# Optimization experiments

Hardware: AMD Instinct MI355X
Metric: run time of the kernel (lower is better)

Reference implementation:

```python
import jax, jax.numpy as jnp
import numpy as np

B, S, D, H = 2, 2048, 1024, 16
DK = D // H
EPS = 1e-5


def setup_inputs() -> dict:
    key = jax.random.key(0)
    ks = jax.random.split(key, 6)
    std = (2.0 / (D + D)) ** 0.5
    return {
        "x": jax.random.normal(ks[0], (B, S, D), dtype=jnp.float32),
        "W_Q": jax.random.normal(ks[1], (D, D), dtype=jnp.float32) * std,
        "W_K": jax.random.normal(ks[2], (D, D), dtype=jnp.float32) * std,
        "W_V": jax.random.normal(ks[3], (D, D), dtype=jnp.float32) * std,
        "W_O": jax.random.normal(ks[4], (D, D), dtype=jnp.float32) * std,
        "gain": jnp.ones((D,), dtype=jnp.float32),
        "positions": jnp.arange(S, dtype=jnp.int64 if jax.config.jax_enable_x64 else jnp.int32),
        "theta": 10000,
        "max_seq_len": 2048,
    }


def rmsnorm(x, gain):
    xf = x.astype(jnp.float32)
    rms = jnp.sqrt(jnp.mean(xf * xf, axis=-1, keepdims=True) + EPS)
    return ((xf / rms) * gain).astype(x.dtype)


def apply_rope(x, sin, cos):
    # x: [..., seq, dk]; sin/cos: [seq, dk//2] broadcast over leading dims
    x_even = x[..., 0::2]
    x_odd = x[..., 1::2]
    r_even = x_even * cos - x_odd * sin
    r_odd = x_odd * cos + x_even * sin
    return jnp.stack([r_even, r_odd], axis=-1).reshape(x.shape)


def reference(x, W_Q, W_K, W_V, W_O, gain, positions, theta, max_seq_len):
    seq_len = x.shape[-2]
    Q = jnp.einsum('od,bsd->bso', W_Q, x)
    K = jnp.einsum('od,bsd->bso', W_K, x)
    V = jnp.einsum('od,bsd->bso', W_V, x)
    # RMSNorm over full d_model BEFORE head split (as in original)
    Q = rmsnorm(Q, gain)
    K = rmsnorm(K, gain)
    # split heads: [b, h, s, dk]
    Q = Q.reshape(*Q.shape[:-1], H, DK).swapaxes(-3, -2)
    K = K.reshape(*K.shape[:-1], H, DK).swapaxes(-3, -2)
    V = V.reshape(*V.shape[:-1], H, DK).swapaxes(-3, -2)
    # RoPE tables
    exponents = 2.0 * jnp.arange(DK // 2, dtype=jnp.float32) / DK
    inv_freq = 1.0 / (jnp.float32(theta) ** exponents)
    angles = positions.astype(jnp.float32)[:, None] * inv_freq[None, :]  # [S, DK//2]
    sin, cos = jnp.sin(angles), jnp.cos(angles)
    Q = apply_rope(Q, sin, cos)
    K = apply_rope(K, sin, cos)
    # causal attention
    scores = jnp.einsum('bhqd,bhkd->bhqk', Q, K) / jnp.sqrt(jnp.float32(DK))
    causal = jnp.tril(jnp.ones((seq_len, seq_len), dtype=bool))
    scores = jnp.where(causal, scores, -jnp.inf)
    attn = jax.nn.softmax(scores, axis=-1)
    out = jnp.einsum('bhqk,bhkd->bhqd', attn, V)
    out = out.swapaxes(-3, -2).reshape(*x.shape[:-1], D)
    return jnp.einsum('of,bsf->bso', W_O, out)
```

## Files before the change

### kernel.cpp

```cpp
#include <hip/hip_runtime.h>
#include <hip/hip_bf16.h>

typedef __attribute__((ext_vector_type(8))) __bf16 bf16x8;
typedef __attribute__((ext_vector_type(4))) __bf16 bf16x4;
typedef __attribute__((ext_vector_type(4))) float  f32x4;

#define S_LEN 2048
#define D_DIM 1024
#define NH    16
#define GK    1024
#define GN    1024

__device__ __forceinline__ float fast_exp2(float x) {
#if __has_builtin(__builtin_amdgcn_exp2f)
  return __builtin_amdgcn_exp2f(x);
#else
  return exp2f(x);
#endif
}

__device__ __forceinline__ void gld_lds16(const void* g, void* l) {
  __builtin_amdgcn_global_load_lds(
      (const __attribute__((address_space(1))) unsigned int*)g,
      (__attribute__((address_space(3))) unsigned int*)l, 16, 0, 0);
}

__global__ __launch_bounds__(256) void cast_all(
    const float* __restrict__ x,  const float* __restrict__ wq, const float* __restrict__ wk,
    const float* __restrict__ wv, const float* __restrict__ wo,
    __bf16* __restrict__ xb, __bf16* __restrict__ wqb, __bf16* __restrict__ wkb,
    __bf16* __restrict__ wvb, __bf16* __restrict__ wob)
{
  const int NTOT = 2 << 20;
  for (int i = blockIdx.x * 256 + threadIdx.x; i < NTOT; i += 1024 * 256) {
    const float* s; __bf16* d; int off;
    if (i < (1 << 20)) { s = x; d = xb; off = i; }
    else {
      const int j = i - (1 << 20);
      const int r = j >> 18; off = j & ((1 << 18) - 1);
      s = (r == 0) ? wq : (r == 1) ? wk : (r == 2) ? wv : wo;
      d = (r == 0) ? wqb : (r == 1) ? wkb : (r == 2) ? wvb : wob;
    }
    float4 v = ((const float4*)s)[off];
    bf16x4 o = { (__bf16)v.x, (__bf16)v.y, (__bf16)v.z, (__bf16)v.w };
    ((bf16x4*)d)[off] = o;
  }
}

__global__ __launch_bounds__(256) void gemm_bt(
    const __bf16* __restrict__ A,
    const __bf16* __restrict__ W0, const __bf16* __restrict__ W1, const __bf16* __restrict__ W2,
    __bf16* __restrict__ C0, __bf16* __restrict__ C1, __bf16* __restrict__ VtOut)
{
  const int mode = blockIdx.z;
  const __bf16* Wm = (mode == 0) ? W0 : (mode == 1) ? W1 : W2;

  __shared__ __align__(16) __bf16 As[128 * 64];
  __shared__ __align__(16) __bf16 Bs[128 * 64];

  const int tid  = threadIdx.x;
  const int lane = tid & 63;
  const int w    = tid >> 6;
  const int wr   = w >> 1, wc = w & 1;
  const int lm   = lane & 15, qd = lane >> 4;
  const int m0 = blockIdx.y * 128, n0 = blockIdx.x * 128;

  const __bf16* ap[4]; const __bf16* bp[4]; int lo[4];
  #pragma unroll
  for (int j = 0; j < 4; j++) {
    const int c = tid + 256 * j;
    const int r = c >> 3, cpos = c & 7;
    const int g = (cpos ^ (r & 7)) * 8;
    ap[j] = A  + (size_t)(m0 + r) * GK + g;
    bp[j] = Wm + (size_t)(n0 + r) * GK + g;
    lo[j] = c * 8;
  }

  const int sw = lm & 7;

  f32x4 zero = {0.f, 0.f, 0.f, 0.f};
  f32x4 acc[4][4];
  #pragma unroll
  for (int i = 0; i < 4; i++)
    #pragma unroll
    for (int j = 0; j < 4; j++) acc[i][j] = zero;

  for (int k0 = 0; k0 < GK; k0 += 64) {
    #pragma unroll
    for (int j = 0; j < 4; j++) {
      gld_lds16(ap[j] + k0, &As[lo[j]]);
      gld_lds16(bp[j] + k0, &Bs[lo[j]]);
    }
    __syncthreads();
    #pragma unroll
    for (int half = 0; half < 2; half++) {
      const int cph = ((qd + 4 * half) ^ sw) * 8;
      bf16x8 af[4], bfv[4];
      #pragma unroll
      for (int i = 0; i < 4; i++) af[i]  = *(const bf16x8*)&As[(wr * 64 + i * 16 + lm) * 64 + cph];
      #pragma unroll
      for (int j = 0; j < 4; j++) bfv[j] = *(const bf16x8*)&Bs[(wc * 64 + j * 16 + lm) * 64 + cph];
      #pragma unroll
      for (int i = 0; i < 4; i++)
        #pragma unroll
        for (int j = 0; j < 4; j++)
          acc[i][j] = __builtin_amdgcn_mfma_f32_16x16x32_bf16(af[i], bfv[j], acc[i][j], 0, 0, 0);
    }
    __syncthreads();
  }

  if (mode < 2) {
    __bf16* C = (mode == 0) ? C0 : C1;
    #pragma unroll
    for (int i = 0; i < 4; i++) {
      const int row = m0 + wr * 64 + i * 16 + qd * 4;
      #pragma unroll
      for (int j = 0; j < 4; j++) {
        const int col = n0 + wc * 64 + j * 16 + lm;
        #pragma unroll
        for (int r = 0; r < 4; r++)
          C[(size_t)(row + r) * GN + col] = (__bf16)acc[i][j][r];
      }
    }
  } else {
    #pragma unroll
    for (int i = 0; i < 4; i++) {
      const int row = m0 + wr * 64 + i * 16 + qd * 4;
      const int b = row >> 11, s = row & (S_LEN - 1);
      #pragma unroll
      for (int j = 0; j < 4; j++) {
        const int col = n0 + wc * 64 + j * 16 + lm;
        const int h = col >> 6, d = col & 63;
        bf16x4 o = { (__bf16)acc[i][j][0], (__bf16)acc[i][j][1],
                     (__bf16)acc[i][j][2], (__bf16)acc[i][j][3] };
        *(bf16x4*)(VtOut + (((size_t)(b * NH + h) * 64 + d) * S_LEN + s)) = o;
      }
    }
  }
}

__global__ __launch_bounds__(256) void gemm_out64(
    const __bf16* __restrict__ A, const __bf16* __restrict__ Wm, float* __restrict__ C)
{
  __shared__ __align__(16) __bf16 As[64 * 64];
  __shared__ __align__(16) __bf16 Bs[128 * 64];

  const int tid  = threadIdx.x;
  const int lane = tid & 63;
  const int w    = tid >> 6;
  const int wr   = w >> 1, wc = w & 1;
  const int lm   = lane & 15, qd = lane >> 4;
  const int m0 = blockIdx.y * 64, n0 = blockIdx.x * 128;

  const __bf16* ap[2]; int loA[2];
  #pragma unroll
  for (int j = 0; j < 2; j++) {
    const int c = tid + 256 * j;
    const int r = c >> 3, cpos = c & 7;
    ap[j] = A + (size_t)(m0 + r) * GK + (cpos ^ (r & 7)) * 8;
    loA[j] = c * 8;
  }
  const __bf16* bp[4]; int loB[4];
  #pragma unroll
  for (int j = 0; j < 4; j++) {
    const int c = tid + 256 * j;
    const int r = c >> 3, cpos = c & 7;
    bp[j] = Wm + (size_t)(n0 + r) * GK + (cpos ^ (r & 7)) * 8;
    loB[j] = c * 8;
  }

  const int sw = lm & 7;

  f32x4 zero = {0.f, 0.f, 0.f, 0.f};
  f32x4 acc[2][4];
  #pragma unroll
  for (int i = 0; i < 2; i++)
    #pragma unroll
    for (int j = 0; j < 4; j++) acc[i][j] = zero;

  for (int k0 = 0; k0 < GK; k0 += 64) {
    #pragma unroll
    for (int j = 0; j < 2; j++) gld_lds16(ap[j] + k0, &As[loA[j]]);
    #pragma unroll
    for (int j = 0; j < 4; j++) gld_lds16(bp[j] + k0, &Bs[loB[j]]);
    __syncthreads();
    #pragma unroll
    for (int half = 0; half < 2; half++) {
      const int cph = ((qd + 4 * half) ^ sw) * 8;
      bf16x8 af[2], bfv[4];
      #pragma unroll
      for (int i = 0; i < 2; i++) af[i]  = *(const bf16x8*)&As[(wr * 32 + i * 16 + lm) * 64 + cph];
      #pragma unroll
      for (int j = 0; j < 4; j++) bfv[j] = *(const bf16x8*)&Bs[(wc * 64 + j * 16 + lm) * 64 + cph];
      #pragma unroll
      for (int i = 0; i < 2; i++)
        #pragma unroll
        for (int j = 0; j < 4; j++)
          acc[i][j] = __builtin_amdgcn_mfma_f32_16x16x32_bf16(af[i], bfv[j], acc[i][j], 0, 0, 0);
    }
    __syncthreads();
  }

  #pragma unroll
  for (int i = 0; i < 2; i++) {
    const int row = m0 + wr * 32 + i * 16 + qd * 4;
    #pragma unroll
    for (int j = 0; j < 4; j++) {
      const int col = n0 + wc * 64 + j * 16 + lm;
      #pragma unroll
      for (int r = 0; r < 4; r++)
        C[(size_t)(row + r) * GN + col] = acc[i][j][r];
    }
  }
}

__global__ __launch_bounds__(256) void norm_rope(
    const __bf16* __restrict__ Qf, const __bf16* __restrict__ Kf,
    const float* __restrict__ gain, const int* __restrict__ positions,
    const int* __restrict__ theta_p,
    __bf16* __restrict__ Qh, __bf16* __restrict__ Kh)
{
  const int row = blockIdx.x;
  const int s = row & (S_LEN - 1), b = row >> 11;
  const int t = threadIdx.x, d0 = t * 4;

  const bf16x4 qv = *(const bf16x4*)(Qf + (size_t)row * D_DIM + d0);
  const bf16x4 kv = *(const bf16x4*)(Kf + (size_t)row * D_DIM + d0);
  const float q0 = (float)qv[0], q1 = (float)qv[1], q2 = (float)qv[2], q3 = (float)qv[3];
  const float k0 = (float)kv[0], k1 = (float)kv[1], k2 = (float)kv[2], k3 = (float)kv[3];

  float sq = q0 * q0 + q1 * q1 + q2 * q2 + q3 * q3;
  float sk = k0 * k0 + k1 * k1 + k2 * k2 + k3 * k3;
  #pragma unroll
  for (int off = 32; off; off >>= 1) { sq += __shfl_xor(sq, off); sk += __shfl_xor(sk, off); }
  __shared__ float red[8];
  const int lane = t & 63, wv = t >> 6;
  if (lane == 0) { red[wv] = sq; red[4 + wv] = sk; }
  __syncthreads();
  sq = red[0] + red[1] + red[2] + red[3];
  sk = red[4] + red[5] + red[6] + red[7];
  const float invq = rsqrtf(sq * (1.0f / 1024.0f) + 1e-5f);
  const float invk = rsqrtf(sk * (1.0f / 1024.0f) + 1e-5f);

  const float4 g = *(const float4*)(gain + d0);
  const float qn0 = q0 * invq * g.x, qn1 = q1 * invq * g.y;
  const float qn2 = q2 * invq * g.z, qn3 = q3 * invq * g.w;
  const float kn0 = k0 * invk * g.x, kn1 = k1 * invk * g.y;
  const float kn2 = k2 * invk * g.z, kn3 = k3 * invk * g.w;

  const float pos = (float)positions[s];
  const float th  = (float)theta_p[0];
  const int idx = d0 & 63, h = d0 >> 6, p0 = idx >> 1;
  const float lg32 = __log2f(th) * (1.0f / 32.0f);
  const float f0 = fast_exp2(-(float)p0 * lg32);
  const float f1 = fast_exp2(-(float)(p0 + 1) * lg32);
  float s0, cc0, s1, cc1;
  __sincosf(pos * f0, &s0, &cc0);
  __sincosf(pos * f1, &s1, &cc1);

  const float qe0 = qn0 * cc0 - qn1 * s0, qo0 = qn1 * cc0 + qn0 * s0;
  const float qe1 = qn2 * cc1 - qn3 * s1, qo1 = qn3 * cc1 + qn2 * s1;
  const float ke0 = kn0 * cc0 - kn1 * s0, ko0 = kn1 * cc0 + kn0 * s0;
  const float ke1 = kn2 * cc1 - kn3 * s1, ko1 = kn3 * cc1 + kn2 * s1;

  const size_t obase = ((size_t)((b * NH + h) * S_LEN + s)) * 64 + idx;
  bf16x4 qo = { (__bf16)qe0, (__bf16)qo0, (__bf16)qe1, (__bf16)qo1 };
  bf16x4 ko = { (__bf16)ke0, (__bf16)ko0, (__bf16)ke1, (__bf16)ko1 };
  *(bf16x4*)(Qh + obase) = qo;
  *(bf16x4*)(Kh + obase) = ko;
}

__global__ __launch_bounds__(256) void attn_fwd(
    const __bf16* __restrict__ Qh, const __bf16* __restrict__ Kh,
    const __bf16* __restrict__ Vt, __bf16* __restrict__ Ob)
{
  const int bid = blockIdx.x;
  const int g   = bid >> 5, gj = g & 7, gs = g >> 3;
  const int qt  = (gs == 0) ? 31 - gj : (gs == 1) ? gj : (gs == 2) ? 23 - gj : 8 + gj;
  const int rr  = bid & 31;
  const int bh  = (rr & 7) * 4 + (rr >> 3);
  const int tid = threadIdx.x, lane = tid & 63, w = tid >> 6;
  const int lm = lane & 15, qd = lane >> 4;

  __shared__ __align__(16) __bf16 smem[8192 + 8192 + 4096];
  __bf16* Ks = smem;
  __bf16* Vs = smem + 8192;
  __bf16* Pw = smem + 16384 + w * 1024;

  const int row0 = qt * 64 + w * 16;
  const size_t qbase = (size_t)bh * S_LEN * 64;
  const bf16x8 aq0 = *(const bf16x8*)(Qh + qbase + (size_t)(row0 + lm) * 64 + qd * 8);
  const bf16x8 aq1 = *(const bf16x8*)(Qh + qbase + (size_t)(row0 + lm) * 64 + 32 + qd * 8);

  const __bf16* Kb = Kh + (size_t)bh * S_LEN * 64;
  const __bf16* Vb = Vt + (size_t)bh * 64 * S_LEN;
  const int c0 = tid, c1 = 256 + tid;
  const int kr0 = c0 >> 3, kr1 = c1 >> 3;
  const int kg0 = ((c0 & 7) ^ (kr0 & 7)) * 8;
  const int kg1 = ((c1 & 7) ^ (kr1 & 7)) * 8;
  const int cpA = (qd ^ (lm & 7)) * 8;
  const int cpB = cpA ^ 32;

  auto stage = [&](int buf, int k0) {
    __bf16* Kd = Ks + buf * 4096;
    __bf16* Vd = Vs + buf * 4096;
    gld_lds16(Kb + (size_t)(k0 + kr0) * 64 + kg0, &Kd[c0 * 8]);
    gld_lds16(Kb + (size_t)(k0 + kr1) * 64 + kg1, &Kd[c1 * 8]);
    gld_lds16(Vb + (size_t)kr0 * S_LEN + k0 + kg0, &Vd[c0 * 8]);
    gld_lds16(Vb + (size_t)kr1 * S_LEN + k0 + kg1, &Vd[c1 * 8]);
  };

  const float SC2 = 0.125f * 1.44269504089f;
  const float OFF = 12.0f;
  f32x4 zero = {0.f, 0.f, 0.f, 0.f};
  float l[4] = {0.f, 0.f, 0.f, 0.f};
  f32x4 o[4];
  #pragma unroll
  for (int jb = 0; jb < 4; jb++) o[jb] = zero;

  stage(0, 0);

  const int rowg = row0 + qd * 4;
  const int pxor = qd * 4;

  for (int kt = 0; kt <= qt; ++kt) {
    const int cur = kt & 1;
    __syncthreads();
    if (kt < qt) stage(cur ^ 1, (kt + 1) * 64);

    const __bf16* Kc = Ks + cur * 4096;
    const __bf16* Vc = Vs + cur * 4096;
    const int k0 = kt * 64;

    float p[4][4];
    const bool diag = (kt == qt);
    #pragma unroll
    for (int kb = 0; kb < 4; kb++) {
      const int krow = (kb * 16 + lm) * 64;
      const bf16x8 bk0 = *(const bf16x8*)&Kc[krow + cpA];
      const bf16x8 bk1 = *(const bf16x8*)&Kc[krow + cpB];
      f32x4 sc = zero;
      sc = __builtin_amdgcn_mfma_f32_16x16x32_bf16(aq0, bk0, sc, 0, 0, 0);
      sc = __builtin_amdgcn_mfma_f32_16x16x32_bf16(aq1, bk1, sc, 0, 0, 0);
      if (diag) {
        const int colg = k0 + kb * 16 + lm;
        #pragma unroll
        for (int r = 0; r < 4; r++) {
          const float e = fast_exp2(fmaf(sc[r], SC2, -OFF));
          p[kb][r] = (colg <= rowg + r) ? e : 0.f;
          l[r] += p[kb][r];
        }
      } else {
        #pragma unroll
        for (int r = 0; r < 4; r++) {
          p[kb][r] = fast_exp2(fmaf(sc[r], SC2, -OFF));
          l[r] += p[kb][r];
        }
      }
    }

    #pragma unroll
    for (int kb = 0; kb < 4; kb++) {
      const int cb = kb * 2 + (lm >> 3), wi = lm & 7;
      #pragma unroll
      for (int r = 0; r < 4; r++) {
        const int prow = pxor + r;
        Pw[prow * 64 + ((cb ^ (prow & 7)) << 3) + wi] = (__bf16)p[kb][r];
      }
    }

    const bf16x8 ap0 = *(const bf16x8*)&Pw[lm * 64 + cpA];
    const bf16x8 ap1 = *(const bf16x8*)&Pw[lm * 64 + cpB];
    #pragma unroll
    for (int jb = 0; jb < 4; jb++) {
      const int vrow = (jb * 16 + lm) * 64;
      const bf16x8 bv0 = *(const bf16x8*)&Vc[vrow + cpA];
      const bf16x8 bv1 = *(const bf16x8*)&Vc[vrow + cpB];
      o[jb] = __builtin_amdgcn_mfma_f32_16x16x32_bf16(ap1, bv1,
              __builtin_amdgcn_mfma_f32_16x16x32_bf16(ap0, bv0, o[jb], 0, 0, 0), 0, 0, 0);
    }
  }

  const int b = bh >> 4, h = bh & 15;
  #pragma unroll
  for (int r = 0; r < 4; r++) {
    float lr = l[r];
    #pragma unroll
    for (int off = 8; off; off >>= 1) lr += __shfl_xor(lr, off);
    const float inv = 1.0f / lr;
    const size_t base = ((size_t)(b * S_LEN + rowg + r)) * D_DIM + h * 64;
    #pragma unroll
    for (int jb = 0; jb < 4; jb++)
      Ob[base + jb * 16 + lm] = (__bf16)(o[jb][r] * inv);
  }
}

extern "C" void kernel_launch(void* const* d_in, const int* in_sizes, int n_in,
                              void* d_out, int out_size, void* d_ws, size_t ws_size,
                              hipStream_t stream)
{
  (void)in_sizes; (void)n_in; (void)out_size; (void)ws_size;
  const float* x    = (const float*)d_in[0];
  const float* WQ   = (const float*)d_in[1];
  const float* WK   = (const float*)d_in[2];
  const float* WV   = (const float*)d_in[3];
  const float* WO   = (const float*)d_in[4];
  const float* gain = (const float*)d_in[5];
  const int* positions = (const int*)d_in[6];
  const int* theta     = (const int*)d_in[7];
  float* out = (float*)d_out;

  char* ws = (char*)d_ws;
  const size_t MB = 1024 * 1024;
  __bf16* xb  = (__bf16*)(ws + 0);
  __bf16* WQb = (__bf16*)(ws + 8  * MB);
  __bf16* WKb = (__bf16*)(ws + 10 * MB);
  __bf16* WVb = (__bf16*)(ws + 12 * MB);
  __bf16* WOb = (__bf16*)(ws + 14 * MB);
  __bf16* Qfb = (__bf16*)(ws + 16 * MB);
  __bf16* Kfb = (__bf16*)(ws + 24 * MB);
  __bf16* Vt  = (__bf16*)(ws + 32 * MB);
  __bf16* Qh  = (__bf16*)(ws + 40 * MB);
  __bf16* Kh  = (__bf16*)(ws + 48 * MB);
  __bf16* Ob  = (__bf16*)(ws + 56 * MB);

  cast_all<<<1024, 256, 0, stream>>>(x, WQ, WK, WV, WO, xb, WQb, WKb, WVb, WOb);
  gemm_bt<<<dim3(8, 32, 3), 256, 0, stream>>>(xb, WQb, WKb, WVb, Qfb, Kfb, Vt);
  norm_rope<<<4096, 256, 0, stream>>>(Qfb, Kfb, gain, positions, theta, Qh, Kh);
  attn_fwd<<<1024, 256, 0, stream>>>(Qh, Kh, Vt, Ob);
  gemm_out64<<<dim3(8, 64), 256, 0, stream>>>(Ob, WOb, out);
}
```

Baseline: 190.8 us.

## Shrink QKV GEMM tiles to 64x128 and remap blocks for XCD-aware L2 locality

The QKV projection GEMM now uses 64x128 tiles instead of 128x128, which doubles the block count to 1536 so more of the GPU's compute units are filled. Both GEMMs switch to a 1D grid where the low three bits of the block id pick a region of the output, so blocks that land on the same XCD tend to share rows of A and columns of W in L2. Launch bounds now ask for 6 blocks per CU to raise occupancy. The cost is lower arithmetic intensity per tile, meaning more LDS and global traffic per FLOP, and the occupancy hint may limit registers.

```diff
diff --git a/kernel.cpp b/kernel.cpp
--- a/kernel.cpp
+++ b/kernel.cpp
@@ -47,15 +47,21 @@
   }
 }
 
-__global__ __launch_bounds__(256) void gemm_bt(
+__global__ __launch_bounds__(256, 6) void gemm_qkv(
     const __bf16* __restrict__ A,
     const __bf16* __restrict__ W0, const __bf16* __restrict__ W1, const __bf16* __restrict__ W2,
     __bf16* __restrict__ C0, __bf16* __restrict__ C1, __bf16* __restrict__ VtOut)
 {
-  const int mode = blockIdx.z;
+  const int bid = blockIdx.x;
+  const int e = bid & 7, mg = e >> 1, ng = e & 1;
+  const int q = bid >> 3;
+  const int mode = q % 3;
+  const int t = q / 3;
+  const int m0 = (mg * 16 + (t & 15)) * 64;
+  const int n0 = (ng * 4 + (t >> 4)) * 128;
   const __bf16* Wm = (mode == 0) ? W0 : (mode == 1) ? W1 : W2;
 
-  __shared__ __align__(16) __bf16 As[128 * 64];
+  __shared__ __align__(16) __bf16 As[64 * 64];
   __shared__ __align__(16) __bf16 Bs[128 * 64];
 
   const int tid  = threadIdx.x;
@@ -63,45 +69,49 @@
   const int w    = tid >> 6;
   const int wr   = w >> 1, wc = w & 1;
   const int lm   = lane & 15, qd = lane >> 4;
-  const int m0 = blockIdx.y * 128, n0 = blockIdx.x * 128;
-
-  const __bf16* ap[4]; const __bf16* bp[4]; int lo[4];
+
+  const __bf16* ap[2]; int loA[2];
+  #pragma unroll
+  for (int j = 0; j < 2; j++) {
+    const int c = tid + 256 * j;
+    const int r = c >> 3, cpos = c & 7;
+    ap[j] = A + (size_t)(m0 + r) * GK + (cpos ^ (r & 7)) * 8;
+    loA[j] = c * 8;
+  }
+  const __bf16* bp[4]; int loB[4];
   #pragma unroll
   for (int j = 0; j < 4; j++) {
     const int c = tid + 256 * j;
     const int r = c >> 3, cpos = c & 7;
-    const int g = (cpos ^ (r & 7)) * 8;
-    ap[j] = A  + (size_t)(m0 + r) * GK + g;
-    bp[j] = Wm + (size_t)(n0 + r) * GK + g;
-    lo[j] = c * 8;
+    bp[j] = Wm + (size_t)(n0 + r) * GK + (cpos ^ (r & 7)) * 8;
+    loB[j] = c * 8;
   }
 
   const int sw = lm & 7;
 
   f32x4 zero = {0.f, 0.f, 0.f, 0.f};
-  f32x4 acc[4][4];
-  #pragma unroll
-  for (int i = 0; i < 4; i++)
+  f32x4 acc[2][4];
+  #pragma unroll
+  for (int i = 0; i < 2; i++)
     #pragma unroll
     for (int j = 0; j < 4; j++) acc[i][j] = zero;
 
   for (int k0 = 0; k0 < GK; k0 += 64) {
     #pragma unroll
-    for (int j = 0; j < 4; j++) {
-      gld_lds16(ap[j] + k0, &As[lo[j]]);
-      gld_lds16(bp[j] + k0, &Bs[lo[j]]);
-    }
+    for (int j = 0; j < 2; j++) gld_lds16(ap[j] + k0, &As[loA[j]]);
+    #pragma unroll
+    for (int j = 0; j < 4; j++) gld_lds16(bp[j] + k0, &Bs[loB[j]]);
     __syncthreads();
     #pragma unroll
     for (int half = 0; half < 2; half++) {
       const int cph = ((qd + 4 * half) ^ sw) * 8;
-      bf16x8 af[4], bfv[4];
-      #pragma unroll
-      for (int i = 0; i < 4; i++) af[i]  = *(const bf16x8*)&As[(wr * 64 + i * 16 + lm) * 64 + cph];
+      bf16x8 af[2], bfv[4];
+      #pragma unroll
+      for (int i = 0; i < 2; i++) af[i]  = *(const bf16x8*)&As[(wr * 32 + i * 16 + lm) * 64 + cph];
       #pragma unroll
       for (int j = 0; j < 4; j++) bfv[j] = *(const bf16x8*)&Bs[(wc * 64 + j * 16 + lm) * 64 + cph];
       #pragma unroll
-      for (int i = 0; i < 4; i++)
+      for (int i = 0; i < 2; i++)
         #pragma unroll
         for (int j = 0; j < 4; j++)
           acc[i][j] = __builtin_amdgcn_mfma_f32_16x16x32_bf16(af[i], bfv[j], acc[i][j], 0, 0, 0);
@@ -112,8 +122,8 @@
   if (mode < 2) {
     __bf16* C = (mode == 0) ? C0 : C1;
     #pragma unroll
-    for (int i = 0; i < 4; i++) {
-      const int row = m0 + wr * 64 + i * 16 + qd * 4;
+    for (int i = 0; i < 2; i++) {
+      const int row = m0 + wr * 32 + i * 16 + qd * 4;
       #pragma unroll
       for (int j = 0; j < 4; j++) {
         const int col = n0 + wc * 64 + j * 16 + lm;
@@ -124,8 +134,8 @@
     }
   } else {
     #pragma unroll
-    for (int i = 0; i < 4; i++) {
-      const int row = m0 + wr * 64 + i * 16 + qd * 4;
+    for (int i = 0; i < 2; i++) {
+      const int row = m0 + wr * 32 + i * 16 + qd * 4;
       const int b = row >> 11, s = row & (S_LEN - 1);
       #pragma unroll
       for (int j = 0; j < 4; j++) {
@@ -139,9 +149,15 @@
   }
 }
 
-__global__ __launch_bounds__(256) void gemm_out64(
+__global__ __launch_bounds__(256, 6) void gemm_out64(
     const __bf16* __restrict__ A, const __bf16* __restrict__ Wm, float* __restrict__ C)
 {
+  const int bid = blockIdx.x;
+  const int e = bid & 7, mg = e >> 1, ng = e & 1;
+  const int q = bid >> 3;
+  const int m0 = (mg * 16 + (q & 15)) * 64;
+  const int n0 = (ng * 4 + (q >> 4)) * 128;
+
   __shared__ __align__(16) __bf16 As[64 * 64];
   __shared__ __align__(16) __bf16 Bs[128 * 64];
 
@@ -150,7 +166,6 @@
   const int w    = tid >> 6;
   const int wr   = w >> 1, wc = w & 1;
   const int lm   = lane & 15, qd = lane >> 4;
-  const int m0 = blockIdx.y * 64, n0 = blockIdx.x * 128;
 
   const __bf16* ap[2]; int loA[2];
   #pragma unroll
@@ -425,8 +440,8 @@
   __bf16* Ob  = (__bf16*)(ws + 56 * MB);
 
   cast_all<<<1024, 256, 0, stream>>>(x, WQ, WK, WV, WO, xb, WQb, WKb, WVb, WOb);
-  gemm_bt<<<dim3(8, 32, 3), 256, 0, stream>>>(xb, WQb, WKb, WVb, Qfb, Kfb, Vt);
+  gemm_qkv<<<1536, 256, 0, stream>>>(xb, WQb, WKb, WVb, Qfb, Kfb, Vt);
   norm_rope<<<4096, 256, 0, stream>>>(Qfb, Kfb, gain, positions, theta, Qh, Kh);
   attn_fwd<<<1024, 256, 0, stream>>>(Qh, Kh, Vt, Ob);
-  gemm_out64<<<dim3(8, 64), 256, 0, stream>>>(Ob, WOb, out);
-}
+  gemm_out64<<<512, 256, 0, stream>>>(Ob, WOb, out);
+}
```

After: 178.5 us. 6.4% less time.
